# Kernel optimization log

Measured on AMD Instinct MI355X. Metric: run time of the kernel, lower is better.

Reference implementation:

```python
import jax, jax.numpy as jnp
import numpy as np

B, S, E, H = 2, 4096, 512, 8
D = E // H  # head_dim = 64


def setup_inputs() -> dict:
    key = jax.random.key(0)
    ks = jax.random.split(key, 5)
    s = E ** -0.5
    return {
        "x": jax.random.normal(ks[0], (B, S, E), dtype=jnp.float32),
        "w_qkv": jax.random.normal(ks[1], (E, 3 * E), dtype=jnp.float32) * s,
        "b_qkv": jnp.zeros((3 * E,), dtype=jnp.float32),
        "w_out": jax.random.normal(ks[2], (E, E), dtype=jnp.float32) * s,
        "b_out": jnp.zeros((E,), dtype=jnp.float32),
    }


def reference(x, w_qkv, b_qkv, w_out, b_out):
    # qkv projection: [B,S,3E] -> [3,B,H,S,D]
    qkv = (x @ w_qkv + b_qkv).reshape(B, S, 3, H, D).transpose(2, 0, 3, 1, 4)
    q, k, v = qkv[0], qkv[1], qkv[2]
    # full score matrix [B,H,S,S] (faithful to the unfused torch impl)
    attn = jnp.einsum("bhqd,bhkd->bhqk", q, k) * (D ** -0.5)
    attn = jax.nn.softmax(attn, axis=-1)
    # dropout in eval mode -> identity (deterministic reference)
    out = jnp.einsum("bhqk,bhkd->bhqd", attn, v)  # [B,H,S,D]
    out = out.transpose(0, 2, 1, 3).reshape(B, S, E)
    return out @ w_out + b_out
```

## Files before the change

### kernel.cpp

```cpp
#include <hip/hip_runtime.h>
#include <hip/hip_bf16.h>

typedef __attribute__((ext_vector_type(8))) short bf16x8;
typedef __attribute__((ext_vector_type(4))) float f32x4;

#define MFMA16 __builtin_amdgcn_mfma_f32_16x16x32_bf16

__device__ __forceinline__ unsigned short f2bf(float f) {
  unsigned int u = __builtin_bit_cast(unsigned int, f);
  u += 0x7FFFu + ((u >> 16) & 1u);
  return (unsigned short)(u >> 16);
}

__device__ __forceinline__ void load_lds16(const void* g, void* l) {
  __builtin_amdgcn_global_load_lds(
      (const __attribute__((address_space(1))) unsigned int*)g,
      (__attribute__((address_space(3))) unsigned int*)l, 16, 0, 0);
}

__global__ __launch_bounds__(256) void prep_kernel(
    const float* __restrict__ x, const float* __restrict__ wqkv,
    const float* __restrict__ wout, unsigned short* __restrict__ xb,
    unsigned short* __restrict__ wqkvT, unsigned short* __restrict__ woutT) {
  int blk = blockIdx.x;
  int t = threadIdx.x;
  if (blk < 4096) {
    int i = (blk * 256 + t) * 4;
    float4 v = *(const float4*)(x + i);
    ushort4 o;
    o.x = f2bf(v.x); o.y = f2bf(v.y); o.z = f2bf(v.z); o.w = f2bf(v.w);
    *(ushort4*)(xb + i) = o;
  } else if (blk < 4864) {
    int u = ((blk - 4096) * 256 + t) * 4;
    int k = u / 1536, n = u % 1536;
    float4 v = *(const float4*)(wqkv + (size_t)k * 1536 + n);
    wqkvT[(size_t)(n + 0) * 512 + k] = f2bf(v.x);
    wqkvT[(size_t)(n + 1) * 512 + k] = f2bf(v.y);
    wqkvT[(size_t)(n + 2) * 512 + k] = f2bf(v.z);
    wqkvT[(size_t)(n + 3) * 512 + k] = f2bf(v.w);
  } else {
    int u = ((blk - 4864) * 256 + t) * 4;
    int k = u >> 9, n = u & 511;
    float4 v = *(const float4*)(wout + (size_t)k * 512 + n);
    woutT[(size_t)(n + 0) * 512 + k] = f2bf(v.x);
    woutT[(size_t)(n + 1) * 512 + k] = f2bf(v.y);
    woutT[(size_t)(n + 2) * 512 + k] = f2bf(v.z);
    woutT[(size_t)(n + 3) * 512 + k] = f2bf(v.w);
  }
}

__global__ __launch_bounds__(256, 2) void qkv_gemm(
    const unsigned short* __restrict__ xb, const unsigned short* __restrict__ bt,
    const float* __restrict__ bias, unsigned short* __restrict__ qout,
    unsigned short* __restrict__ ksw, unsigned short* __restrict__ vtsw) {
  __shared__ unsigned short SH[16384];
  const int t = threadIdx.x;
  const int lane = t & 63;
  const int llo = lane & 15, lhi = lane >> 4;
  const int w = t >> 6, wr = w >> 1, wc = w & 1;
  const int m0 = blockIdx.x * 128, n0 = blockIdx.y * 128;

  f32x4 acc[4][4];
#pragma unroll
  for (int i = 0; i < 4; ++i)
#pragma unroll
    for (int j = 0; j < 4; ++j) acc[i][j] = (f32x4){0.f, 0.f, 0.f, 0.f};

  const int r0 = t >> 2;
  const int sb = (t & 3) * 16;

  auto stage = [&](int k0, int buf) {
    const char* ga = (const char*)xb + (size_t)(m0 + r0) * 1024 + k0 * 2 + sb;
    const char* gb = (const char*)bt + (size_t)(n0 + r0) * 1024 + k0 * 2 + sb;
    char* la = (char*)SH + buf * 8192;
    char* lb = (char*)SH + 16384 + buf * 8192;
    load_lds16(ga, la + t * 16);
    load_lds16(ga + 64 * 1024, la + 4096 + t * 16);
    load_lds16(gb, lb + t * 16);
    load_lds16(gb + 64 * 1024, lb + 4096 + t * 16);
  };

  stage(0, 0);
  __syncthreads();

  int cur = 0;
  for (int k0 = 0; k0 < 512; k0 += 32) {
    if (k0 + 32 < 512) stage(k0 + 32, cur ^ 1);

    const unsigned short* usA = SH + cur * 4096;
    const unsigned short* usB = SH + 8192 + cur * 4096;
    bf16x8 af[4], bf[4];
#pragma unroll
    for (int mi = 0; mi < 4; ++mi)
      af[mi] = *(const bf16x8*)(usA + (wr * 64 + mi * 16 + llo) * 32 + lhi * 8);
#pragma unroll
    for (int ni = 0; ni < 4; ++ni)
      bf[ni] = *(const bf16x8*)(usB + (wc * 64 + ni * 16 + llo) * 32 + lhi * 8);
#pragma unroll
    for (int mi = 0; mi < 4; ++mi)
#pragma unroll
      for (int ni = 0; ni < 4; ++ni)
        acc[mi][ni] = MFMA16(af[mi], bf[ni], acc[mi][ni], 0, 0, 0);
    __syncthreads();
    cur ^= 1;
  }

  const int sec = n0 >> 9;
  const int hbase = (n0 >> 6) & 7;
#pragma unroll
  for (int ni = 0; ni < 4; ++ni) {
    int lcol = wc * 64 + ni * 16 + llo;
    float bv = bias[n0 + lcol];
#pragma unroll
    for (int mi = 0; mi < 4; ++mi) {
#pragma unroll
      for (int r = 0; r < 4; ++r) {
        int rowm = wr * 64 + mi * 16 + lhi * 4 + r;
        float val = acc[mi][ni][r] + bv;
        unsigned short bits;
        int idx;
        if (sec == 0) {
          bits = f2bf(val * 0.18033688f);
          idx = rowm * 128 + (lcol ^ ((rowm & 15) << 3));
        } else if (sec == 1) {
          bits = f2bf(val);
          idx = rowm * 128 + (lcol ^ ((rowm & 15) << 3));
        } else {
          bits = f2bf(val);
          int u64k = rowm & 63;
          int c = u64k >> 4, u = u64k & 15;
          int kperm = ((c >> 1) << 5) + ((u >> 2) << 3) + ((c & 1) << 2) + (u & 3);
          int ktile = rowm >> 6;
          idx = lcol * 128 + ((ktile * 64 + kperm) ^ ((lcol & 15) << 3));
        }
        SH[idx] = bits;
      }
    }
  }
  __syncthreads();

  const int b = m0 >> 12;
  if (sec == 0) {
#pragma unroll
    for (int j = 0; j < 8; ++j) {
      int cidx = j * 256 + t;
      int dc = cidx & 7, srow = (cidx >> 3) & 127, h2 = cidx >> 10;
      int bh = b * 8 + hbase + h2;
      int s = (m0 & 4095) + srow;
      bf16x8 v = *(const bf16x8*)(SH + srow * 128 +
                                  ((h2 * 64 + dc * 8) ^ ((srow & 15) << 3)));
      *(bf16x8*)(qout + ((size_t)bh * 4096 + s) * 64 + dc * 8) = v;
    }
  } else if (sec == 1) {
#pragma unroll
    for (int j = 0; j < 8; ++j) {
      int cidx = j * 256 + t;
      int dc = cidx & 7, srow = (cidx >> 3) & 127, h2 = cidx >> 10;
      int bh = b * 8 + hbase + h2;
      int s = (m0 & 4095) + srow;
      bf16x8 v = *(const bf16x8*)(SH + srow * 128 +
                                  ((h2 * 64 + dc * 8) ^ ((srow & 15) << 3)));
      size_t byte = (size_t)bh * 524288 + (size_t)(s >> 6) * 8192 +
                    (size_t)(s & 63) * 128 + ((dc * 16) ^ ((s & 7) << 4));
      *(bf16x8*)((char*)ksw + byte) = v;
    }
  } else {
#pragma unroll
    for (int j = 0; j < 8; ++j) {
      int cidx = j * 256 + t;
      int dc = cidx & 7, drow = (cidx >> 3) & 63;
      int ktile = (cidx >> 9) & 1, h2 = cidx >> 10;
      int bh = b * 8 + hbase + h2;
      int lcol = h2 * 64 + drow;
      bf16x8 v = *(const bf16x8*)(SH + lcol * 128 +
                                  ((ktile * 64 + dc * 8) ^ ((lcol & 15) << 3)));
      size_t byte = (size_t)bh * 524288 +
                    (size_t)(((m0 & 4095) >> 6) + ktile) * 8192 +
                    (size_t)drow * 128 + ((dc * 16) ^ ((drow & 7) << 4));
      *(bf16x8*)((char*)vtsw + byte) = v;
    }
  }
}

__global__ __launch_bounds__(256, 4) void attn_kernel(
    const unsigned short* __restrict__ qp, const unsigned short* __restrict__ ksw,
    const unsigned short* __restrict__ vtsw, unsigned short* __restrict__ aout) {
  __shared__ unsigned short Ks[2][4096];
  __shared__ unsigned short Vts[2][4096];

  const int t = threadIdx.x, lane = t & 63, w = t >> 6;
  const int llo = lane & 15, lhi = lane >> 4;

  const int wg = blockIdx.x + (blockIdx.y << 6);
  const int pidx = ((wg & 7) << 7) + (wg >> 3);
  const int bh = pidx >> 6;
  const int q0 = (pidx & 63) * 64 + w * 16;

  bf16x8 qf[2];
#pragma unroll
  for (int f = 0; f < 2; ++f) {
    int row = q0 + llo;
    int d = f * 32 + lhi * 8;
    qf[f] = *(const bf16x8*)(qp + ((size_t)bh * 4096 + row) * 64 + d);
  }

  float lpart = 0.f;
  f32x4 o[4];
#pragma unroll
  for (int di = 0; di < 4; ++di) o[di] = (f32x4){0.f, 0.f, 0.f, 0.f};

  const char* kbase = (const char*)ksw + (size_t)bh * 524288;
  const char* vbase = (const char*)vtsw + (size_t)bh * 524288;

  bf16x8 pf[2];

  auto stage_tile = [&](const char* g, char* d) {
    load_lds16(g + t * 16, d + t * 16);
    load_lds16(g + 4096 + t * 16, d + 4096 + t * 16);
  };

  auto qkt = [&](f32x4 (&sc)[4], const char* kbuf) {
    __builtin_amdgcn_s_setprio(1);
#pragma unroll
    for (int c = 0; c < 4; ++c) {
      int krow = c * 16 + llo;
      int sw = (krow & 7) << 4;
      bf16x8 kf0 = *(const bf16x8*)(kbuf + krow * 128 + ((lhi * 16) ^ sw));
      bf16x8 kf1 = *(const bf16x8*)(kbuf + krow * 128 + ((lhi * 16 + 64) ^ sw));
      sc[c] = MFMA16(kf0, qf[0], (f32x4){0.f, 0.f, 0.f, 0.f}, 0, 0, 0);
      sc[c] = MFMA16(kf1, qf[1], sc[c], 0, 0, 0);
    }
    __builtin_amdgcn_s_setprio(0);
  };

  auto softmax_pack = [&](f32x4 (&sc)[4]) {
    float e[4][4];
#pragma unroll
    for (int c = 0; c < 4; ++c)
#pragma unroll
      for (int r = 0; r < 4; ++r) {
        e[c][r] = __builtin_amdgcn_exp2f(sc[c][r]);
        lpart += e[c][r];
      }
#pragma unroll
    for (int f = 0; f < 2; ++f) {
      bf16x8 pvv;
#pragma unroll
      for (int j = 0; j < 8; ++j)
        pvv[j] = __builtin_bit_cast(short,
                     __float2bfloat16(e[2 * f + (j >> 2)][j & 3]));
      pf[f] = pvv;
    }
  };

  auto pv_accum = [&](const char* vbuf) {
    __builtin_amdgcn_s_setprio(1);
#pragma unroll
    for (int f = 0; f < 2; ++f)
#pragma unroll
      for (int di = 0; di < 4; ++di) {
        int vrow = di * 16 + llo;
        int byte = vrow * 128 + ((lhi * 16 + f * 64) ^ ((vrow & 7) << 4));
        bf16x8 vf = *(const bf16x8*)(vbuf + byte);
        o[di] = MFMA16(pf[f], vf, o[di], 0, 0, 0);
      }
    __builtin_amdgcn_s_setprio(0);
  };

  stage_tile(kbase, (char*)&Ks[0][0]);
  stage_tile(vbase, (char*)&Vts[0][0]);
  stage_tile(kbase + 8192, (char*)&Ks[1][0]);
  __syncthreads();

  f32x4 scA[4], scB[4];
  qkt(scA, (const char*)&Ks[0][0]);
  __syncthreads();

  for (int kt = 0; kt < 62; kt += 2) {
    stage_tile(kbase + (size_t)(kt + 2) * 8192, (char*)&Ks[0][0]);
    stage_tile(vbase + (size_t)(kt + 1) * 8192, (char*)&Vts[1][0]);
    qkt(scB, (const char*)&Ks[1][0]);
    softmax_pack(scA);
    pv_accum((const char*)&Vts[0][0]);
    __syncthreads();
    stage_tile(kbase + (size_t)(kt + 3) * 8192, (char*)&Ks[1][0]);
    stage_tile(vbase + (size_t)(kt + 2) * 8192, (char*)&Vts[0][0]);
    qkt(scA, (const char*)&Ks[0][0]);
    softmax_pack(scB);
    pv_accum((const char*)&Vts[1][0]);
    __syncthreads();
  }

  stage_tile(vbase + (size_t)63 * 8192, (char*)&Vts[1][0]);
  qkt(scB, (const char*)&Ks[1][0]);
  softmax_pack(scA);
  pv_accum((const char*)&Vts[0][0]);
  __syncthreads();
  softmax_pack(scB);
  pv_accum((const char*)&Vts[1][0]);

  float linv[4];
  {
    float s = lpart;
    s += __shfl_xor(s, 16, 64);
    s += __shfl_xor(s, 32, 64);
#pragma unroll
    for (int r = 0; r < 4; ++r)
      linv[r] = 1.f / __shfl(s, lhi * 4 + r, 64);
  }

  int b = bh >> 3, h = bh & 7;
#pragma unroll
  for (int di = 0; di < 4; ++di)
#pragma unroll
    for (int r = 0; r < 4; ++r) {
      int s = q0 + lhi * 4 + r;
      int d = di * 16 + llo;
      float val = o[di][r] * linv[r];
      aout[((size_t)b * 4096 + s) * 512 + h * 64 + d] = f2bf(val);
    }
}

__global__ __launch_bounds__(256, 2) void out_gemm(
    const unsigned short* __restrict__ ab, const unsigned short* __restrict__ bt,
    const float* __restrict__ bias, float* __restrict__ out) {
  __shared__ unsigned short As[2][128 * 32];
  __shared__ unsigned short Bs[2][64 * 32];
  const int t = threadIdx.x;
  const int lane = t & 63;
  const int llo = lane & 15, lhi = lane >> 4;
  const int w = t >> 6;
  const int m0 = blockIdx.x * 128, n0 = blockIdx.y * 64;

  f32x4 acc[2][4];
#pragma unroll
  for (int i = 0; i < 2; ++i)
#pragma unroll
    for (int j = 0; j < 4; ++j) acc[i][j] = (f32x4){0.f, 0.f, 0.f, 0.f};

  const int r0 = t >> 2;
  const int sb = (t & 3) * 16;

  auto stage = [&](int k0, int buf) {
    const char* ga = (const char*)ab + (size_t)(m0 + r0) * 1024 + k0 * 2 + sb;
    const char* gb = (const char*)bt + (size_t)(n0 + r0) * 1024 + k0 * 2 + sb;
    load_lds16(ga, (char*)&As[buf][0] + t * 16);
    load_lds16(ga + 64 * 1024, (char*)&As[buf][0] + 4096 + t * 16);
    load_lds16(gb, (char*)&Bs[buf][0] + t * 16);
  };

  stage(0, 0);
  __syncthreads();

  int cur = 0;
  for (int k0 = 0; k0 < 512; k0 += 32) {
    if (k0 + 32 < 512) stage(k0 + 32, cur ^ 1);

    bf16x8 af[2], bf[4];
#pragma unroll
    for (int mi = 0; mi < 2; ++mi)
      af[mi] = *(const bf16x8*)(&As[cur][0] + (w * 32 + mi * 16 + llo) * 32 + lhi * 8);
#pragma unroll
    for (int ni = 0; ni < 4; ++ni)
      bf[ni] = *(const bf16x8*)(&Bs[cur][0] + (ni * 16 + llo) * 32 + lhi * 8);
#pragma unroll
    for (int mi = 0; mi < 2; ++mi)
#pragma unroll
      for (int ni = 0; ni < 4; ++ni)
        acc[mi][ni] = MFMA16(af[mi], bf[ni], acc[mi][ni], 0, 0, 0);
    __syncthreads();
    cur ^= 1;
  }

#pragma unroll
  for (int ni = 0; ni < 4; ++ni) {
    int col = n0 + ni * 16 + llo;
    float bv = bias[col];
#pragma unroll
    for (int mi = 0; mi < 2; ++mi) {
      int rowb = m0 + w * 32 + mi * 16 + lhi * 4;
#pragma unroll
      for (int r = 0; r < 4; ++r)
        out[(size_t)(rowb + r) * 512 + col] = acc[mi][ni][r] + bv;
    }
  }
}

extern "C" void kernel_launch(void* const* d_in, const int* in_sizes, int n_in,
                              void* d_out, int out_size, void* d_ws, size_t ws_size,
                              hipStream_t stream) {
  const float* x = (const float*)d_in[0];
  const float* wqkv = (const float*)d_in[1];
  const float* bqkv = (const float*)d_in[2];
  const float* wout = (const float*)d_in[3];
  const float* bout = (const float*)d_in[4];
  float* out = (float*)d_out;

  char* ws = (char*)d_ws;
  unsigned short* xb    = (unsigned short*)(ws + 0);
  unsigned short* wqkvT = (unsigned short*)(ws + 8388608);
  unsigned short* woutT = (unsigned short*)(ws + 9961472);
  unsigned short* qb    = (unsigned short*)(ws + 10485760);
  unsigned short* ksw   = (unsigned short*)(ws + 18874368);
  unsigned short* vtsw  = (unsigned short*)(ws + 27262976);
  unsigned short* ab    = (unsigned short*)(ws + 35651584);
  (void)ws_size; (void)in_sizes; (void)n_in; (void)out_size;

  prep_kernel<<<5120, 256, 0, stream>>>(x, wqkv, wout, xb, wqkvT, woutT);
  qkv_gemm<<<dim3(64, 12), 256, 0, stream>>>(xb, wqkvT, bqkv, qb, ksw, vtsw);
  attn_kernel<<<dim3(64, 16), 256, 0, stream>>>(qb, ksw, vtsw, ab);
  out_gemm<<<dim3(64, 8), 256, 0, stream>>>(ab, woutT, bout, out);
}
```

Before: 135.9 us.

## Split attention key tiles across wave pairs, each wave handling two query strips

The attention kernel's four waves are now arranged as two query groups of 32 rows, each split into two halves of the 64-key tile. Each K and V fragment read from LDS is reused across two query strips, which halves LDS fragment reads per MFMA. The two key-half partial outputs and row sums are combined through LDS at the end. This adds an epilogue reduction with an extra barrier and raises register use for the doubled accumulators.

```diff
diff --git a/kernel.cpp b/kernel.cpp
--- a/kernel.cpp
+++ b/kernel.cpp
@@ -190,80 +190,90 @@
 
   const int t = threadIdx.x, lane = t & 63, w = t >> 6;
   const int llo = lane & 15, lhi = lane >> 4;
+  const int g = w >> 1;
+  const int kh = w & 1;
 
   const int wg = blockIdx.x + (blockIdx.y << 6);
   const int pidx = ((wg & 7) << 7) + (wg >> 3);
   const int bh = pidx >> 6;
-  const int q0 = (pidx & 63) * 64 + w * 16;
-
-  bf16x8 qf[2];
-#pragma unroll
-  for (int f = 0; f < 2; ++f) {
-    int row = q0 + llo;
-    int d = f * 32 + lhi * 8;
-    qf[f] = *(const bf16x8*)(qp + ((size_t)bh * 4096 + row) * 64 + d);
-  }
-
-  float lpart = 0.f;
-  f32x4 o[4];
-#pragma unroll
-  for (int di = 0; di < 4; ++di) o[di] = (f32x4){0.f, 0.f, 0.f, 0.f};
+  const int q0 = (pidx & 63) * 64;
+  const int qb = q0 + g * 32;
+
+  bf16x8 qf[2][2];
+#pragma unroll
+  for (int strip = 0; strip < 2; ++strip)
+#pragma unroll
+    for (int f = 0; f < 2; ++f) {
+      int row = qb + strip * 16 + llo;
+      int d = f * 32 + lhi * 8;
+      qf[strip][f] = *(const bf16x8*)(qp + ((size_t)bh * 4096 + row) * 64 + d);
+    }
+
+  float lpart[2] = {0.f, 0.f};
+  f32x4 o[2][4];
+#pragma unroll
+  for (int strip = 0; strip < 2; ++strip)
+#pragma unroll
+    for (int di = 0; di < 4; ++di) o[strip][di] = (f32x4){0.f, 0.f, 0.f, 0.f};
 
   const char* kbase = (const char*)ksw + (size_t)bh * 524288;
   const char* vbase = (const char*)vtsw + (size_t)bh * 524288;
 
   bf16x8 pf[2];
 
-  auto stage_tile = [&](const char* g, char* d) {
-    load_lds16(g + t * 16, d + t * 16);
-    load_lds16(g + 4096 + t * 16, d + 4096 + t * 16);
-  };
-
-  auto qkt = [&](f32x4 (&sc)[4], const char* kbuf) {
+  auto stage_tile = [&](const char* gsrc, char* d) {
+    load_lds16(gsrc + t * 16, d + t * 16);
+    load_lds16(gsrc + 4096 + t * 16, d + 4096 + t * 16);
+  };
+
+  auto qkt = [&](f32x4 (&sc)[2][2], const char* kbuf) {
     __builtin_amdgcn_s_setprio(1);
 #pragma unroll
-    for (int c = 0; c < 4; ++c) {
-      int krow = c * 16 + llo;
+    for (int c = 0; c < 2; ++c) {
+      int krow = kh * 32 + c * 16 + llo;
       int sw = (krow & 7) << 4;
       bf16x8 kf0 = *(const bf16x8*)(kbuf + krow * 128 + ((lhi * 16) ^ sw));
       bf16x8 kf1 = *(const bf16x8*)(kbuf + krow * 128 + ((lhi * 16 + 64) ^ sw));
-      sc[c] = MFMA16(kf0, qf[0], (f32x4){0.f, 0.f, 0.f, 0.f}, 0, 0, 0);
-      sc[c] = MFMA16(kf1, qf[1], sc[c], 0, 0, 0);
+#pragma unroll
+      for (int strip = 0; strip < 2; ++strip) {
+        sc[strip][c] = MFMA16(kf0, qf[strip][0], (f32x4){0.f, 0.f, 0.f, 0.f}, 0, 0, 0);
+        sc[strip][c] = MFMA16(kf1, qf[strip][1], sc[strip][c], 0, 0, 0);
+      }
     }
     __builtin_amdgcn_s_setprio(0);
   };
 
-  auto softmax_pack = [&](f32x4 (&sc)[4]) {
-    float e[4][4];
-#pragma unroll
-    for (int c = 0; c < 4; ++c)
-#pragma unroll
-      for (int r = 0; r < 4; ++r) {
-        e[c][r] = __builtin_amdgcn_exp2f(sc[c][r]);
-        lpart += e[c][r];
-      }
-#pragma unroll
-    for (int f = 0; f < 2; ++f) {
+  auto softmax_pack = [&](f32x4 (&sc)[2][2]) {
+#pragma unroll
+    for (int strip = 0; strip < 2; ++strip) {
+      float e[2][4];
+#pragma unroll
+      for (int c = 0; c < 2; ++c)
+#pragma unroll
+        for (int r = 0; r < 4; ++r) {
+          e[c][r] = __builtin_amdgcn_exp2f(sc[strip][c][r]);
+          lpart[strip] += e[c][r];
+        }
       bf16x8 pvv;
 #pragma unroll
       for (int j = 0; j < 8; ++j)
         pvv[j] = __builtin_bit_cast(short,
-                     __float2bfloat16(e[2 * f + (j >> 2)][j & 3]));
-      pf[f] = pvv;
+                     __float2bfloat16(e[j >> 2][j & 3]));
+      pf[strip] = pvv;
     }
   };
 
   auto pv_accum = [&](const char* vbuf) {
     __builtin_amdgcn_s_setprio(1);
 #pragma unroll
-    for (int f = 0; f < 2; ++f)
-#pragma unroll
-      for (int di = 0; di < 4; ++di) {
-        int vrow = di * 16 + llo;
-        int byte = vrow * 128 + ((lhi * 16 + f * 64) ^ ((vrow & 7) << 4));
-        bf16x8 vf = *(const bf16x8*)(vbuf + byte);
-        o[di] = MFMA16(pf[f], vf, o[di], 0, 0, 0);
-      }
+    for (int di = 0; di < 4; ++di) {
+      int vrow = di * 16 + llo;
+      int byte = vrow * 128 + ((lhi * 16 + kh * 64) ^ ((vrow & 7) << 4));
+      bf16x8 vf = *(const bf16x8*)(vbuf + byte);
+#pragma unroll
+      for (int strip = 0; strip < 2; ++strip)
+        o[strip][di] = MFMA16(pf[strip], vf, o[strip][di], 0, 0, 0);
+    }
     __builtin_amdgcn_s_setprio(0);
   };
 
@@ -272,7 +282,7 @@
   stage_tile(kbase + 8192, (char*)&Ks[1][0]);
   __syncthreads();
 
-  f32x4 scA[4], scB[4];
+  f32x4 scA[2][2], scB[2][2];
   qkt(scA, (const char*)&Ks[0][0]);
   __syncthreads();
 
@@ -299,26 +309,56 @@
   softmax_pack(scB);
   pv_accum((const char*)&Vts[1][0]);
 
-  float linv[4];
-  {
-    float s = lpart;
+  __syncthreads();
+  float* so = (float*)&Ks[0][0];
+  float* sl = (float*)&Vts[0][0];
+
+  float lred[2];
+#pragma unroll
+  for (int strip = 0; strip < 2; ++strip) {
+    float s = lpart[strip];
     s += __shfl_xor(s, 16, 64);
     s += __shfl_xor(s, 32, 64);
-#pragma unroll
-    for (int r = 0; r < 4; ++r)
-      linv[r] = 1.f / __shfl(s, lhi * 4 + r, 64);
-  }
-
-  int b = bh >> 3, h = bh & 7;
-#pragma unroll
-  for (int di = 0; di < 4; ++di)
-#pragma unroll
-    for (int r = 0; r < 4; ++r) {
-      int s = q0 + lhi * 4 + r;
-      int d = di * 16 + llo;
-      float val = o[di][r] * linv[r];
-      aout[((size_t)b * 4096 + s) * 512 + h * 64 + d] = f2bf(val);
-    }
+    lred[strip] = s;
+  }
+
+  if (kh == 1) {
+#pragma unroll
+    for (int strip = 0; strip < 2; ++strip) {
+#pragma unroll
+      for (int di = 0; di < 4; ++di)
+#pragma unroll
+        for (int r = 0; r < 4; ++r) {
+          int srow = strip * 16 + lhi * 4 + r;
+          so[g * 2048 + srow * 64 + di * 16 + llo] = o[strip][di][r];
+        }
+      if (lhi == 0) sl[g * 32 + strip * 16 + llo] = lred[strip];
+    }
+  }
+  __syncthreads();
+  if (kh == 0) {
+    float linv[2][4];
+#pragma unroll
+    for (int strip = 0; strip < 2; ++strip) {
+      float s = lred[strip] + sl[g * 32 + strip * 16 + llo];
+#pragma unroll
+      for (int r = 0; r < 4; ++r)
+        linv[strip][r] = 1.f / __shfl(s, lhi * 4 + r, 64);
+    }
+    int b = bh >> 3, h = bh & 7;
+#pragma unroll
+    for (int strip = 0; strip < 2; ++strip)
+#pragma unroll
+      for (int di = 0; di < 4; ++di)
+#pragma unroll
+        for (int r = 0; r < 4; ++r) {
+          int srow = strip * 16 + lhi * 4 + r;
+          int d = di * 16 + llo;
+          float val = (o[strip][di][r] + so[g * 2048 + srow * 64 + d]) *
+                      linv[strip][r];
+          aout[((size_t)b * 4096 + qb + srow) * 512 + h * 64 + d] = f2bf(val);
+        }
+  }
 }
 
 __global__ __launch_bounds__(256, 2) void out_gemm(
```

New measurement: 199.4 us. +46.8%, slower.
